# Performance work log

Hardware: AMD Instinct MI355X
Metric: run time of the kernel (lower is better)

Reference implementation:

```python
import jax, jax.numpy as jnp
import numpy as np

DELTA = 0.5
WEIGHT = 1.0
W = 1.85 + DELTA  # ego width  (+ safety delta)
H = 4.084 + DELTA  # ego length (+ safety delta)

F = 6          # planning futures
N = 1000000    # gt boxes per future (padded)


def setup_inputs() -> dict:
    key = jax.random.key(0)
    k1, k2, k3 = jax.random.split(key, 3)
    return {
        "sdc_traj_all": jax.random.normal(k1, (1, F, 2), dtype=jnp.float32),
        "sdc_planning_gt": jax.random.normal(k2, (1, F, 3), dtype=jnp.float32),
        "sdc_planning_gt_mask": jnp.ones((1, F, 2), dtype=jnp.float32),
        "future_gt_corners": jax.random.normal(k3, (F, N, 4, 2), dtype=jnp.float32),
        "box_mask": jnp.ones((F, N), dtype=bool),
    }


def _sdc_corners(x, y, theta):
    # local box corners [4,2] (w/2, l/2 pattern as in to_corners)
    local = jnp.array([[W / 2, -H / 2], [W / 2, H / 2],
                       [-W / 2, H / 2], [-W / 2, -H / 2]], dtype=x.dtype)  # [4,2]
    c, s = jnp.cos(theta), jnp.sin(theta)  # [F]
    # rot_mat = [[c, s], [-s, c]]; new_corners = (rot @ local.T + t).T
    rot = jnp.stack([jnp.stack([c, s], -1), jnp.stack([-s, c], -1)], -2)  # [F,2,2]
    corners = jnp.einsum('fij,kj->fki', rot, local)  # [F,4,2]
    return corners + jnp.stack([x, y], -1)[:, None, :]  # [F,4,2]


def reference(sdc_traj_all, sdc_planning_gt, sdc_planning_gt_mask, future_gt_corners, box_mask):
    x = sdc_traj_all[0, :, 0]
    y = sdc_traj_all[0, :, 1]
    theta = sdc_planning_gt[0, :, 2].astype(sdc_traj_all.dtype)
    sdc = _sdc_corners(x, y, theta)  # [F,4,2]

    # ego AABB per future
    xa1 = sdc[..., 0].max(-1)[:, None]  # [F,1]
    ya1 = sdc[..., 1].max(-1)[:, None]
    xa2 = sdc[..., 0].min(-1)[:, None]
    ya2 = sdc[..., 1].min(-1)[:, None]

    # gt boxes AABB per (future, box)
    xb1 = future_gt_corners[..., 0].max(-1)  # [F,N]
    yb1 = future_gt_corners[..., 1].max(-1)
    xb2 = future_gt_corners[..., 0].min(-1)
    yb2 = future_gt_corners[..., 1].min(-1)

    w = jnp.clip(jnp.minimum(xa1, xb1) - jnp.maximum(xa2, xb2), 0)
    h = jnp.clip(jnp.minimum(ya1, yb1) - jnp.maximum(ya2, yb2), 0)
    inter = jnp.where(box_mask, w * h, 0.0)
    return (inter.sum() * WEIGHT).reshape(1)
```

## Files before the change

kernel.cpp:

```cpp
#include <hip/hip_runtime.h>
#include <math.h>

#define NFRAMES 6
#define NBOX    1000000
#define TOTAL   (NFRAMES * NBOX)

#define HALF_W  (2.35f * 0.5f)
#define HALF_H  (4.584f * 0.5f)

__global__ void zero_out_kernel(float* out) { out[0] = 0.0f; }

__global__ __launch_bounds__(256) void CollisionLoss_55327768708655_kernel(
    const float* __restrict__ traj,
    const float* __restrict__ gt,
    const float* __restrict__ corners,
    const int* __restrict__ mask,
    float* __restrict__ out)
{
    __shared__ float s_xa1[NFRAMES], s_ya1[NFRAMES], s_xa2[NFRAMES], s_ya2[NFRAMES];
    if (threadIdx.x < NFRAMES) {
        int f = threadIdx.x;
        float x  = traj[f * 2 + 0];
        float y  = traj[f * 2 + 1];
        float th = gt[f * 3 + 2];
        float c = cosf(th), s = sinf(th);
        float ex = fabsf(c) * HALF_W + fabsf(s) * HALF_H;
        float ey = fabsf(s) * HALF_W + fabsf(c) * HALF_H;
        s_xa1[f] = x + ex;  s_xa2[f] = x - ex;
        s_ya1[f] = y + ey;  s_ya2[f] = y - ey;
    }
    __syncthreads();

    float acc = 0.0f;
    int stride = gridDim.x * blockDim.x;
    for (int i = blockIdx.x * blockDim.x + threadIdx.x; i < TOTAL; i += stride) {
        const float4* p = (const float4*)(corners + (size_t)i * 8);
        float4 a = p[0];
        float4 b = p[1];
        float xb1 = fmaxf(fmaxf(a.x, a.z), fmaxf(b.x, b.z));
        float xb2 = fminf(fminf(a.x, a.z), fminf(b.x, b.z));
        float yb1 = fmaxf(fmaxf(a.y, a.w), fmaxf(b.y, b.w));
        float yb2 = fminf(fminf(a.y, a.w), fminf(b.y, b.w));

        int f = i / NBOX;
        float w = fminf(s_xa1[f], xb1) - fmaxf(s_xa2[f], xb2);
        float h = fminf(s_ya1[f], yb1) - fmaxf(s_ya2[f], yb2);
        w = fmaxf(w, 0.0f);
        h = fmaxf(h, 0.0f);
        float v = w * h;
        acc += mask[i] ? v : 0.0f;
    }

    #pragma unroll
    for (int off = 32; off > 0; off >>= 1)
        acc += __shfl_down(acc, off, 64);

    __shared__ float s_part[4];
    int lane = threadIdx.x & 63;
    int wave = threadIdx.x >> 6;
    if (lane == 0) s_part[wave] = acc;
    __syncthreads();
    if (threadIdx.x == 0) {
        float t = s_part[0] + s_part[1] + s_part[2] + s_part[3];
        atomicAdd(out, t);
    }
}

extern "C" void kernel_launch(void* const* d_in, const int* in_sizes, int n_in,
                              void* d_out, int out_size, void* d_ws, size_t ws_size,
                              hipStream_t stream) {
    const float* traj     = (const float*)d_in[0];
    const float* gt       = (const float*)d_in[1];
    const float* corners  = (const float*)d_in[3];
    const int* mask       = (const int*)d_in[4];
    float* out = (float*)d_out;

    zero_out_kernel<<<1, 1, 0, stream>>>(out);

    CollisionLoss_55327768708655_kernel<<<2048, 256, 0, stream>>>(traj, gt, corners, mask, out);
}
```

Measured before the change: 287.7 us.

## Process four boxes per thread with wide loads and two-pass block reduction

Replaces the grid-stride loop with one-shot threads that each handle four consecutive boxes, issuing eight float4 corner loads and one int4 mask load per thread to raise memory-level parallelism. The per-frame ego AABB is packed into one float4 in shared memory. The global atomicAdd and zeroing kernel are replaced by per-block partials in the workspace plus a single-block finalize kernel, which also makes the sum deterministic. It launches many more blocks (about 5860) and adds a second small kernel launch.

```diff
diff --git a/kernel.cpp b/kernel.cpp
--- a/kernel.cpp
+++ b/kernel.cpp
@@ -5,19 +5,22 @@
 #define NBOX    1000000
 #define TOTAL   (NFRAMES * NBOX)
 
+#define BPT     4
+#define NTHREADS (TOTAL / BPT)
+#define BLOCK   256
+#define NBLOCKS ((NTHREADS + BLOCK - 1) / BLOCK)
+
 #define HALF_W  (2.35f * 0.5f)
 #define HALF_H  (4.584f * 0.5f)
 
-__global__ void zero_out_kernel(float* out) { out[0] = 0.0f; }
-
-__global__ __launch_bounds__(256) void CollisionLoss_55327768708655_kernel(
+__global__ __launch_bounds__(BLOCK) void CollisionLoss_55327768708655_kernel(
     const float* __restrict__ traj,
     const float* __restrict__ gt,
     const float* __restrict__ corners,
-    const int* __restrict__ mask,
-    float* __restrict__ out)
+    const int*   __restrict__ mask,
+    float* __restrict__ partials)
 {
-    __shared__ float s_xa1[NFRAMES], s_ya1[NFRAMES], s_xa2[NFRAMES], s_ya2[NFRAMES];
+    __shared__ float4 s_frame[NFRAMES];
     if (threadIdx.x < NFRAMES) {
         int f = threadIdx.x;
         float x  = traj[f * 2 + 0];
@@ -26,44 +29,67 @@
         float c = cosf(th), s = sinf(th);
         float ex = fabsf(c) * HALF_W + fabsf(s) * HALF_H;
         float ey = fabsf(s) * HALF_W + fabsf(c) * HALF_H;
-        s_xa1[f] = x + ex;  s_xa2[f] = x - ex;
-        s_ya1[f] = y + ey;  s_ya2[f] = y - ey;
+        s_frame[f] = make_float4(x + ex, y + ey, x - ex, y - ey);
     }
     __syncthreads();
 
     float acc = 0.0f;
-    int stride = gridDim.x * blockDim.x;
-    for (int i = blockIdx.x * blockDim.x + threadIdx.x; i < TOTAL; i += stride) {
-        const float4* p = (const float4*)(corners + (size_t)i * 8);
-        float4 a = p[0];
-        float4 b = p[1];
-        float xb1 = fmaxf(fmaxf(a.x, a.z), fmaxf(b.x, b.z));
-        float xb2 = fminf(fminf(a.x, a.z), fminf(b.x, b.z));
-        float yb1 = fmaxf(fmaxf(a.y, a.w), fmaxf(b.y, b.w));
-        float yb2 = fminf(fminf(a.y, a.w), fminf(b.y, b.w));
+    int tid = blockIdx.x * BLOCK + threadIdx.x;
+    if (tid < NTHREADS) {
+        const float4* p = (const float4*)corners + (size_t)tid * (2 * BPT);
+        float4 A[8];
+        #pragma unroll
+        for (int j = 0; j < 8; ++j) A[j] = p[j];
+        int4 m = ((const int4*)mask)[tid];
 
-        int f = i / NBOX;
-        float w = fminf(s_xa1[f], xb1) - fmaxf(s_xa2[f], xb2);
-        float h = fminf(s_ya1[f], yb1) - fmaxf(s_ya2[f], yb2);
-        w = fmaxf(w, 0.0f);
-        h = fmaxf(h, 0.0f);
-        float v = w * h;
-        acc += mask[i] ? v : 0.0f;
+        int f = (tid * BPT) / NBOX;
+        float4 fr = s_frame[f];
+
+        int M[4] = {m.x, m.y, m.z, m.w};
+        #pragma unroll
+        for (int j = 0; j < BPT; ++j) {
+            float4 a = A[2 * j + 0];
+            float4 b = A[2 * j + 1];
+            float xb1 = fmaxf(fmaxf(a.x, a.z), fmaxf(b.x, b.z));
+            float xb2 = fminf(fminf(a.x, a.z), fminf(b.x, b.z));
+            float yb1 = fmaxf(fmaxf(a.y, a.w), fmaxf(b.y, b.w));
+            float yb2 = fminf(fminf(a.y, a.w), fminf(b.y, b.w));
+            float w = fminf(fr.x, xb1) - fmaxf(fr.z, xb2);
+            float h = fminf(fr.y, yb1) - fmaxf(fr.w, yb2);
+            float v = fmaxf(w, 0.0f) * fmaxf(h, 0.0f);
+            acc += M[j] ? v : 0.0f;
+        }
     }
 
     #pragma unroll
     for (int off = 32; off > 0; off >>= 1)
         acc += __shfl_down(acc, off, 64);
 
-    __shared__ float s_part[4];
+    __shared__ float s_part[BLOCK / 64];
     int lane = threadIdx.x & 63;
     int wave = threadIdx.x >> 6;
     if (lane == 0) s_part[wave] = acc;
     __syncthreads();
-    if (threadIdx.x == 0) {
-        float t = s_part[0] + s_part[1] + s_part[2] + s_part[3];
-        atomicAdd(out, t);
-    }
+    if (threadIdx.x == 0)
+        partials[blockIdx.x] = s_part[0] + s_part[1] + s_part[2] + s_part[3];
+}
+
+__global__ __launch_bounds__(BLOCK) void finalize_kernel(
+    const float* __restrict__ partials, float* __restrict__ out)
+{
+    float acc = 0.0f;
+    for (int i = threadIdx.x; i < NBLOCKS; i += BLOCK)
+        acc += partials[i];
+    #pragma unroll
+    for (int off = 32; off > 0; off >>= 1)
+        acc += __shfl_down(acc, off, 64);
+    __shared__ float s_part[BLOCK / 64];
+    int lane = threadIdx.x & 63;
+    int wave = threadIdx.x >> 6;
+    if (lane == 0) s_part[wave] = acc;
+    __syncthreads();
+    if (threadIdx.x == 0)
+        out[0] = s_part[0] + s_part[1] + s_part[2] + s_part[3];
 }
 
 extern "C" void kernel_launch(void* const* d_in, const int* in_sizes, int n_in,
@@ -72,10 +98,11 @@
     const float* traj     = (const float*)d_in[0];
     const float* gt       = (const float*)d_in[1];
     const float* corners  = (const float*)d_in[3];
-    const int* mask       = (const int*)d_in[4];
-    float* out = (float*)d_out;
+    const int*   mask     = (const int*)d_in[4];
+    float* partials       = (float*)d_ws;
+    float* out            = (float*)d_out;
 
-    zero_out_kernel<<<1, 1, 0, stream>>>(out);
-
-    CollisionLoss_55327768708655_kernel<<<2048, 256, 0, stream>>>(traj, gt, corners, mask, out);
+    CollisionLoss_55327768708655_kernel<<<NBLOCKS, BLOCK, 0, stream>>>(
+        traj, gt, corners, mask, partials);
+    finalize_kernel<<<1, BLOCK, 0, stream>>>(partials, out);
 }
```

Result: no change. 288.9 us (median of 2 runs) (+0.4%).
